# Performance work log

Measured on AMD Instinct MI355X. Metric: run time of the kernel, lower is better.

Reference implementation:

```python
import jax, jax.numpy as jnp
import numpy as np
from jax import lax

K = 3; PAD = 1; STR = 1; DIL = 1; DG = 16; MRM = 10.0


def _conv3(x, w, b):
    y = lax.conv_general_dilated(x, w, (1, 1), ((PAD, PAD), (PAD, PAD)),
                                 dimension_numbers=('NCHW', 'OIHW', 'NCHW'))
    return y + b[None, :, None, None]


def _leaky(x):
    return jnp.where(x >= 0, x, 0.1 * x)


def _bilinear_gather(img, py, px):
    # img: [B, dg, cg, H, W]; py, px: [B, dg, KK, H, W] sampling coords
    B, dg, cg, H, W = img.shape
    KK = py.shape[2]
    y0f = jnp.floor(py); x0f = jnp.floor(px)
    wy = py - y0f; wx = px - x0f          # bilinear fractions (grad flows via py/px)
    y0 = y0f.astype(jnp.int32); x0 = x0f.astype(jnp.int32)
    y1 = y0 + 1; x1 = x0 + 1
    imgf = img.reshape(B * dg, cg, H * W)

    def gather(yi, xi):
        valid = ((yi >= 0) & (yi < H) & (xi >= 0) & (xi < W)).astype(img.dtype)
        idx = jnp.clip(yi, 0, H - 1) * W + jnp.clip(xi, 0, W - 1)
        idxf = idx.reshape(B * dg, KK * H * W)
        v = jax.vmap(lambda im, ix: im[:, ix])(imgf, idxf)  # [B*dg, cg, KK*H*W]
        v = v.reshape(B, dg, cg, KK, H, W)
        return v * valid[:, :, None]  # zero padding outside image

    w00 = ((1 - wy) * (1 - wx))[:, :, None]
    w01 = ((1 - wy) * wx)[:, :, None]
    w10 = (wy * (1 - wx))[:, :, None]
    w11 = (wy * wx)[:, :, None]
    return (gather(y0, x0) * w00 + gather(y0, x1) * w01 +
            gather(y1, x0) * w10 + gather(y1, x1) * w11)


def reference(x, extra_feat, flow, w1, b1, w2, b2, w3, b3, weight):
    B, C, H, W = x.shape
    KK = K * K
    cg = C // DG
    P = DG * KK
    # offset/mask generating convnet
    h = _leaky(_conv3(extra_feat, w1, b1))
    h = _leaky(_conv3(h, w2, b2))
    o = _conv3(h, w3, b3)                       # [B, 3*P, H, W]
    o1, o2, m = jnp.split(o, 3, axis=1)
    off = MRM * jnp.tanh(jnp.concatenate([o1, o2], axis=1))  # [B, 2P, H, W]
    flow_yx = flow[:, ::-1]                      # flip(1): (x,y)->(y,x)
    off = off + jnp.tile(flow_yx, (1, P, 1, 1))
    off = off.reshape(B, DG, KK, 2, H, W)        # pair p=(g,k): channel 2p=y, 2p+1=x
    off_y = off[:, :, :, 0]
    off_x = off[:, :, :, 1]
    mask = jax.nn.sigmoid(m).reshape(B, DG, KK, H, W)

    ki = jnp.arange(KK)
    ky = (ki // K).astype(x.dtype) * DIL - PAD   # kernel row offsets
    kx = (ki % K).astype(x.dtype) * DIL - PAD
    base_h = jnp.arange(H, dtype=x.dtype) * STR
    base_w = jnp.arange(W, dtype=x.dtype) * STR
    py = base_h[None, None, None, :, None] + ky[None, None, :, None, None] + off_y
    px = base_w[None, None, None, None, :] + kx[None, None, :, None, None] + off_x

    img = x.reshape(B, DG, cg, H, W)
    val = _bilinear_gather(img, py, px) * mask[:, :, None]  # [B,dg,cg,KK,H,W]
    wk = weight.reshape(weight.shape[0], DG, cg, KK)
    # modulated deformable conv accumulate (bias=None in original forward)
    return jnp.einsum('bgckhw,ogck->bohw', val, wk)


def setup_inputs() -> dict:
    key = jax.random.key(0)
    ks = jax.random.split(key, 10)
    B, C, H, W = 2, 64, 128, 128
    OFFC = 3 * K * K * DG  # 432
    return {
        'x': jax.random.normal(ks[0], (B, C, H, W), jnp.float32),
        'extra_feat': jax.random.normal(ks[1], (B, 2 * C, H, W), jnp.float32),
        'flow': jax.random.normal(ks[2], (B, 2, H, W), jnp.float32),
        'w1': jax.random.normal(ks[3], (C, 2 * C, 3, 3), jnp.float32) * 0.05,
        'b1': jnp.zeros((C,), jnp.float32),
        'w2': jax.random.normal(ks[4], (C, C, 3, 3), jnp.float32) * 0.05,
        'b2': jnp.zeros((C,), jnp.float32),
        'w3': jax.random.normal(ks[5], (OFFC, C, 3, 3), jnp.float32) * 0.01,
        'b3': jnp.zeros((OFFC,), jnp.float32),
        'weight': jax.random.normal(ks[6], (C, C, 3, 3), jnp.float32) * 0.05,
    }
```

## Files before the change

kernel.cpp:

```cpp
#include <hip/hip_runtime.h>
#include <math.h>

constexpr int B_   = 2;
constexpr int C_   = 64;
constexpr int H_   = 128;
constexpr int W_   = 128;
constexpr int HW_  = H_ * W_;
constexpr int DG_  = 16;
constexpr int KK_  = 9;
constexpr int CG_  = 4;
constexpr int OFFC_ = 3 * KK_ * DG_;
constexpr int R_   = C_ * KK_;
constexpr int WP_  = 130;
constexpr int HWP_ = WP_ * WP_;

typedef _Float16 half8 __attribute__((ext_vector_type(8)));
typedef _Float16 half4 __attribute__((ext_vector_type(4)));
typedef float floatx4 __attribute__((ext_vector_type(4)));

__device__ __forceinline__ void gl_lds16(const _Float16* g, _Float16* l)
{
    __builtin_amdgcn_global_load_lds(
        (const __attribute__((address_space(1))) void*)g,
        (__attribute__((address_space(3))) void*)l, 16, 0, 0);
}

__device__ __forceinline__ int afrag_src(int c)
{
    const int cmf = c >> 6, cq = (c >> 4) & 3, cl = c & 15;
    return (cmf * 16 + cl) * 32 + cq * 8;
}

template <int OC, int CIN>
__global__ __launch_bounds__(256) void prep_wA_k(
    const float* __restrict__ w, _Float16* __restrict__ wA)
{
    constexpr int CH = CIN / 32;
    const int j = blockIdx.x * 256 + threadIdx.x;
    if (j >= 9 * CH * OC * 32) return;
    const int slab = j / (OC * 32);
    const int rem  = j - slab * (OC * 32);
    const int oc   = rem >> 5;
    const int jj   = rem & 31;
    const int t    = slab / CH;
    const int h    = slab - t * CH;
    const int ic   = h * 32 + jj;
    wA[j] = (_Float16)w[(size_t)oc * (CIN * 9) + ic * 9 + t];
}

__global__ __launch_bounds__(256) void prep_wkA_k(
    const float* __restrict__ wk, _Float16* __restrict__ wkA)
{
    const int j = blockIdx.x * 256 + threadIdx.x;
    if (j >= 18 * 64 * 32) return;
    const int s   = j >> 11;
    const int rem = j & 2047;
    const int oc  = rem >> 5;
    const int jj  = rem & 31;
    const int k   = s >> 1;
    const int gc  = (s & 1) * 32 + jj;
    wkA[j] = (_Float16)wk[(size_t)oc * R_ + gc * 9 + k];
}

template <int CC>
__global__ __launch_bounds__(256) void nchw2slabpad_f16_k(
    const float* __restrict__ in, _Float16* __restrict__ outh)
{
    const int pix = blockIdx.x * 256 + threadIdx.x;
    const int b   = blockIdx.y;
    const int yp  = pix >> 7;
    const int xp  = pix & (W_ - 1);
    const float* ib = in + (size_t)b * CC * HW_ + pix;
#pragma unroll
    for (int c0 = 0; c0 < CC; c0 += 8) {
        half8 v;
#pragma unroll
        for (int j = 0; j < 8; ++j)
            v[j] = (_Float16)ib[(size_t)(c0 + j) * HW_];
        const int slab = c0 >> 5;
        *(half8*)&outh[((size_t)(slab * B_ + b) * HWP_
                        + (size_t)(yp + 1) * WP_ + (xp + 1)) * 32 + (c0 & 31)] = v;
    }
}

__global__ __launch_bounds__(256) void nchw2gx_f16_k(
    const float* __restrict__ in, _Float16* __restrict__ outh)
{
    const int pix = blockIdx.x * 256 + threadIdx.x;
    const int b   = blockIdx.y;
    const float* ib = in + (size_t)b * C_ * HW_ + pix;
#pragma unroll
    for (int g = 0; g < DG_; ++g) {
        half4 v;
#pragma unroll
        for (int c = 0; c < 4; ++c)
            v[c] = (_Float16)ib[(size_t)(g * 4 + c) * HW_];
        *(half4*)&outh[((size_t)(b * DG_ + g) * HW_ + pix) * 4] = v;
    }
}

__global__ __launch_bounds__(256, 2) void conv1_mfma_k(
    const _Float16* __restrict__ inp, const _Float16* __restrict__ wA,
    const float* __restrict__ bias, _Float16* __restrict__ outp)
{
    __shared__ __align__(16) _Float16 Asm[2 * 4096];

    const int tid  = threadIdx.x;
    const int lane = tid & 63;
    const int wv   = tid >> 6;
    const int l15  = lane & 15;
    const int quad = lane >> 4;

    const int zx   = blockIdx.x;
    const int row  = zx >> 1;
    const int b    = row >> 7;
    const int y    = row & 127;
    const int px0  = (zx & 1) * 64 + wv * 16;

    const int sA = afrag_src(tid);

    floatx4 acc[4];
#pragma unroll
    for (int mf = 0; mf < 4; ++mf)
        acc[mf] = (floatx4){0.f, 0.f, 0.f, 0.f};

    half8 Bf[2][2];

    gl_lds16(wA + 0 * 2048 + sA, Asm + 0 * 2048 + tid * 8);
    gl_lds16(wA + 1 * 2048 + sA, Asm + 1 * 2048 + tid * 8);
#pragma unroll
    for (int j = 0; j < 2; ++j)
        Bf[0][j] = *(const half8*)&inp[
            ((size_t)(j * B_ + b) * HWP_ + (size_t)(y + 0) * WP_
             + (px0 + l15 + 0)) * 32 + quad * 8];
    __syncthreads();

#pragma unroll
    for (int p = 0; p < 18; ++p) {
        const int cur = p & 1, nxt = cur ^ 1;
        if (p < 17) {
            const int ks0 = 2 * p + 2;
            const int t = ks0 >> 2;
            const int h0 = ks0 & 3;
            const int dy = t / 3, dx = t % 3;
#pragma unroll
            for (int j = 0; j < 2; ++j) {
                gl_lds16(wA + (size_t)(ks0 + j) * 2048 + sA,
                         Asm + (nxt * 2 + j) * 2048 + tid * 8);
                Bf[nxt][j] = *(const half8*)&inp[
                    ((size_t)((h0 + j) * B_ + b) * HWP_ + (size_t)(y + dy) * WP_
                     + (px0 + l15 + dx)) * 32 + quad * 8];
            }
        }
#pragma unroll
        for (int j = 0; j < 2; ++j) {
            const _Float16* abase = Asm + (cur * 2 + j) * 2048 + lane * 8;
#pragma unroll
            for (int mf = 0; mf < 4; ++mf) {
                const half8 afr = *(const half8*)&abase[mf * 512];
                acc[mf] = __builtin_amdgcn_mfma_f32_16x16x32_f16(afr, Bf[cur][j], acc[mf], 0, 0, 0);
            }
        }
        __syncthreads();
    }

#pragma unroll
    for (int mf = 0; mf < 4; ++mf) {
        const int oc4 = mf * 16 + quad * 4;
        const float4 b4 = *(const float4*)&bias[oc4];
        half4 v4;
#pragma unroll
        for (int reg = 0; reg < 4; ++reg) {
            float r = acc[mf][reg] + ((const float*)&b4)[reg];
            r = (r >= 0.f) ? r : 0.1f * r;
            v4[reg] = (_Float16)r;
        }
        *(half4*)&outp[((size_t)((oc4 >> 5) * B_ + b) * HWP_
                        + (size_t)(y + 1) * WP_ + (px0 + l15 + 1)) * 32 + (oc4 & 31)] = v4;
    }
}

__global__ __launch_bounds__(256, 2) void conv2_mfma_k(
    const _Float16* __restrict__ inp, const _Float16* __restrict__ wA,
    const float* __restrict__ bias, _Float16* __restrict__ outp)
{
    __shared__ __align__(16) _Float16 Asm[18 * 2048];

    const int tid  = threadIdx.x;
    const int lane = tid & 63;
    const int wv   = tid >> 6;
    const int l15  = lane & 15;
    const int quad = lane >> 4;

    const int zx   = blockIdx.x;
    const int row  = zx >> 1;
    const int b    = row >> 7;
    const int y    = row & 127;
    const int px0  = (zx & 1) * 64 + wv * 16;

    const int sA = afrag_src(tid);

#pragma unroll
    for (int s = 0; s < 18; ++s)
        gl_lds16(wA + (size_t)s * 2048 + sA, Asm + s * 2048 + tid * 8);

    floatx4 acc[4];
#pragma unroll
    for (int mf = 0; mf < 4; ++mf)
        acc[mf] = (floatx4){0.f, 0.f, 0.f, 0.f};

    half8 Bf[2];
    Bf[0] = *(const half8*)&inp[
        ((size_t)(0 * B_ + b) * HWP_ + (size_t)(y + 0) * WP_
         + (px0 + l15 + 0)) * 32 + quad * 8];
    __syncthreads();

#pragma unroll
    for (int ks = 0; ks < 18; ++ks) {
        const int cur = ks & 1, nxt = cur ^ 1;
        if (ks < 17) {
            const int ks1 = ks + 1;
            const int t = ks1 >> 1, h = ks1 & 1;
            const int dy = t / 3, dx = t % 3;
            Bf[nxt] = *(const half8*)&inp[
                ((size_t)(h * B_ + b) * HWP_ + (size_t)(y + dy) * WP_
                 + (px0 + l15 + dx)) * 32 + quad * 8];
        }
        const _Float16* abase = Asm + ks * 2048 + lane * 8;
#pragma unroll
        for (int mf = 0; mf < 4; ++mf) {
            const half8 afr = *(const half8*)&abase[mf * 512];
            acc[mf] = __builtin_amdgcn_mfma_f32_16x16x32_f16(afr, Bf[cur], acc[mf], 0, 0, 0);
        }
    }

#pragma unroll
    for (int mf = 0; mf < 4; ++mf) {
        const int oc4 = mf * 16 + quad * 4;
        const float4 b4 = *(const float4*)&bias[oc4];
        half4 v4;
#pragma unroll
        for (int reg = 0; reg < 4; ++reg) {
            float r = acc[mf][reg] + ((const float*)&b4)[reg];
            r = (r >= 0.f) ? r : 0.1f * r;
            v4[reg] = (_Float16)r;
        }
        *(half4*)&outp[((size_t)((oc4 >> 5) * B_ + b) * HWP_
                        + (size_t)(y + 1) * WP_ + (px0 + l15 + 1)) * 32 + (oc4 & 31)] = v4;
    }
}

__global__ __launch_bounds__(256, 2) void conv3_mfma_k(
    const _Float16* __restrict__ h2p, const _Float16* __restrict__ w3A,
    const float* __restrict__ bias, const float* __restrict__ flow,
    _Float16* __restrict__ omh)
{
    __shared__ __align__(16) _Float16 Smem[144 * 132];
    _Float16* Asm = Smem;
    _Float16* Lds = Smem;

    const int tid  = threadIdx.x;
    const int lane = tid & 63;
    const int wv   = tid >> 6;
    const int l15  = lane & 15;
    const int quad = lane >> 4;

    const int row = blockIdx.x;
    const int b   = row >> 7;
    const int y   = row & 127;
    const int m0  = blockIdx.y * 144;
    const int px0 = wv * 32;

    const int c0 = wv * 64 + lane;
    const int c1 = 256 + c0;
    const int c2 = 512 + lane;
    const int s0 = afrag_src(c0), s1 = afrag_src(c1), s2 = afrag_src(c2);

    floatx4 acc[9][2];
#pragma unroll
    for (int mf = 0; mf < 9; ++mf)
#pragma unroll
        for (int nf = 0; nf < 2; ++nf)
            acc[mf][nf] = (floatx4){0.f, 0.f, 0.f, 0.f};

    half8 Bf[2][2][2];

    {
#pragma unroll
        for (int j = 0; j < 2; ++j) {
            const _Float16* asrc = w3A + ((size_t)j * OFFC_ + m0) * 32;
            _Float16* adst = Asm + j * 4608;
            gl_lds16(asrc + s0, adst + c0 * 8);
            gl_lds16(asrc + s1, adst + c1 * 8);
            if (wv == 0) gl_lds16(asrc + s2, adst + c2 * 8);
#pragma unroll
            for (int nf = 0; nf < 2; ++nf)
                Bf[0][j][nf] = *(const half8*)&h2p[
                    ((size_t)(j * B_ + b) * HWP_ + (size_t)(y + 0) * WP_
                     + (px0 + nf * 16 + l15 + 0)) * 32 + quad * 8];
        }
    }
    __syncthreads();

#pragma unroll
    for (int p = 0; p < 9; ++p) {
        const int cur = p & 1, nxt = cur ^ 1;
        if (p < 8) {
            const int t = p + 1;
            const int dy = t / 3, dx = t % 3;
#pragma unroll
            for (int j = 0; j < 2; ++j) {
                const int ks = 2 * t + j;
                const _Float16* asrc = w3A + ((size_t)ks * OFFC_ + m0) * 32;
                _Float16* adst = Asm + (nxt * 2 + j) * 4608;
                gl_lds16(asrc + s0, adst + c0 * 8);
                gl_lds16(asrc + s1, adst + c1 * 8);
                if (wv == 0) gl_lds16(asrc + s2, adst + c2 * 8);
#pragma unroll
                for (int nf = 0; nf < 2; ++nf)
                    Bf[nxt][j][nf] = *(const half8*)&h2p[
                        ((size_t)(j * B_ + b) * HWP_ + (size_t)(y + dy) * WP_
                         + (px0 + nf * 16 + l15 + dx)) * 32 + quad * 8];
            }
        }
#pragma unroll
        for (int j = 0; j < 2; ++j) {
            const _Float16* abase = Asm + (cur * 2 + j) * 4608 + lane * 8;
#pragma unroll
            for (int mf = 0; mf < 9; ++mf) {
                const half8 afr = *(const half8*)&abase[mf * 512];
                acc[mf][0] = __builtin_amdgcn_mfma_f32_16x16x32_f16(afr, Bf[cur][j][0], acc[mf][0], 0, 0, 0);
                acc[mf][1] = __builtin_amdgcn_mfma_f32_16x16x32_f16(afr, Bf[cur][j][1], acc[mf][1], 0, 0, 0);
            }
        }
        __syncthreads();
    }

    const bool is_off = (blockIdx.y < 2);
    float flY[2], flX[2];
#pragma unroll
    for (int nf = 0; nf < 2; ++nf) {
        const int px = px0 + nf * 16 + l15;
        if (is_off) {
            flY[nf] = flow[(size_t)(b * 2 + 1) * HW_ + y * W_ + px];
            flX[nf] = flow[(size_t)(b * 2 + 0) * HW_ + y * W_ + px];
        }
    }
#pragma unroll
    for (int mf = 0; mf < 9; ++mf) {
        const float4 b4 = *(const float4*)&bias[m0 + mf * 16 + quad * 4];
#pragma unroll
        for (int nf = 0; nf < 2; ++nf) {
            const int px = px0 + nf * 16 + l15;
#pragma unroll
            for (int reg = 0; reg < 4; ++reg) {
                const int ocl = mf * 16 + quad * 4 + reg;
                float val = acc[mf][nf][reg] + ((const float*)&b4)[reg];
                if (is_off) {
                    const int slot = reg & 1;
                    const float fl = slot ? flX[nf] : flY[nf];
                    const float e = __expf(2.f * val);
                    val = 10.f * (1.f - __fdividef(2.f, e + 1.f)) + fl;
                } else {
                    val = __fdividef(1.f, 1.f + __expf(-val));
                }
                Lds[ocl * 132 + px] = (_Float16)val;
            }
        }
    }
    __syncthreads();

#pragma unroll
    for (int it = 0; it < 18; ++it) {
        const int j4 = it * 256 + tid;
        const int r  = j4 >> 5;
        const int c4 = j4 & 31;
        const int oc = m0 + r;
        int g, k, slot;
        if (oc < 2 * DG_ * KK_) {
            g = oc / 18;
            const int rem = oc - g * 18;
            k = rem >> 1;
            slot = rem & 1;
        } else {
            const int c = oc - 2 * DG_ * KK_;
            g = c / 9;
            k = c - g * 9;
            slot = 2;
        }
        const half4 hv = *(const half4*)&Lds[r * 132 + c4 * 4];
        *(half4*)&omh[((size_t)((b * DG_ * KK_ + g * KK_ + k) * 3 + slot)) * HW_
                      + y * W_ + c4 * 4] = hv;
    }
}

__global__ __launch_bounds__(256) void gather_k(
    const _Float16* __restrict__ xg, const _Float16* __restrict__ omh,
    _Float16* __restrict__ valh)
{
    const int tid = threadIdx.x;
    const int pix = blockIdx.x * 256 + tid;
    const int zy  = blockIdx.y;
    const int b   = zy / KK_;
    const int k   = zy - b * KK_;
    const int yp  = pix >> 7;
    const int xp  = pix & (W_ - 1);
    const float fy = (float)(yp + (k / 3) - 1);
    const float fx = (float)(xp + (k % 3) - 1);

    half4 rec[16];
#pragma unroll
    for (int g = 0; g < DG_; ++g) {
        const size_t obase = ((size_t)((b * DG_ + g) * KK_ + k) * 3) * HW_ + pix;
        const float oy = (float)omh[obase];
        const float ox = (float)omh[obase + HW_];
        const float m  = (float)omh[obase + 2 * HW_];

        const float py = fy + oy;
        const float px = fx + ox;
        const float y0f = floorf(py);
        const float x0f = floorf(px);
        const float wy = py - y0f;
        const float wx = px - x0f;
        const int y0 = (int)y0f, x0 = (int)x0f;
        const int y1 = y0 + 1,  x1 = x0 + 1;
        const bool vy0 = ((unsigned)y0 < (unsigned)H_);
        const bool vy1 = ((unsigned)y1 < (unsigned)H_);
        const bool vx0 = ((unsigned)x0 < (unsigned)W_);
        const bool vx1 = ((unsigned)x1 < (unsigned)W_);
        const float w00 = vy0 && vx0 ? (1.f - wy) * (1.f - wx) : 0.f;
        const float w01 = vy0 && vx1 ? (1.f - wy) * wx         : 0.f;
        const float w10 = vy1 && vx0 ? wy * (1.f - wx)         : 0.f;
        const float w11 = vy1 && vx1 ? wy * wx                 : 0.f;
        const int i00 = (vy0 && vx0) ? y0 * W_ + x0 : 0;
        const int i01 = (vy0 && vx1) ? y0 * W_ + x1 : 0;
        const int i10 = (vy1 && vx0) ? y1 * W_ + x0 : 0;
        const int i11 = (vy1 && vx1) ? y1 * W_ + x1 : 0;

        const _Float16* xb = xg + (size_t)(b * DG_ + g) * HW_ * 4;
        const half4 p00 = *(const half4*)&xb[(size_t)i00 * 4];
        const half4 p01 = *(const half4*)&xb[(size_t)i01 * 4];
        const half4 p10 = *(const half4*)&xb[(size_t)i10 * 4];
        const half4 p11 = *(const half4*)&xb[(size_t)i11 * 4];

        half4 v4;
#pragma unroll
        for (int c = 0; c < CG_; ++c) {
            float v = w00 * (float)p00[c] + w01 * (float)p01[c]
                    + w10 * (float)p10[c] + w11 * (float)p11[c];
            v4[c] = (_Float16)(v * m);
        }
        rec[g] = v4;
    }

    _Float16* r0 = &valh[((size_t)((2 * k) * B_ + b) * HW_ + pix) * 32];
    _Float16* r1 = &valh[((size_t)((2 * k + 1) * B_ + b) * HW_ + pix) * 32];
#pragma unroll
    for (int j = 0; j < 4; ++j) {
        half8 w0, w1;
#pragma unroll
        for (int c = 0; c < 4; ++c) {
            w0[c]     = rec[2 * j][c];
            w0[c + 4] = rec[2 * j + 1][c];
            w1[c]     = rec[8 + 2 * j][c];
            w1[c + 4] = rec[9 + 2 * j][c];
        }
        *(half8*)&r0[j * 8] = w0;
        *(half8*)&r1[j * 8] = w1;
    }
}

__global__ __launch_bounds__(256, 2) void einsum_mfma_k(
    const _Float16* __restrict__ valh, const _Float16* __restrict__ wkA,
    float* __restrict__ out)
{
    __shared__ __align__(16) _Float16 Smem[18 * 2048];
    float* Lds = (float*)Smem;

    const int tid  = threadIdx.x;
    const int lane = tid & 63;
    const int wv   = tid >> 6;
    const int l15  = lane & 15;
    const int quad = lane >> 4;

    const int pixg0 = blockIdx.x * 64 + wv * 16;
    const int b     = pixg0 >> 14;
    const int pix0  = pixg0 & (HW_ - 1);

    const int sA = afrag_src(tid);

#pragma unroll
    for (int s = 0; s < 18; ++s)
        gl_lds16(wkA + (size_t)s * 2048 + sA, Smem + s * 2048 + tid * 8);

    floatx4 acc[4];
#pragma unroll
    for (int mf = 0; mf < 4; ++mf)
        acc[mf] = (floatx4){0.f, 0.f, 0.f, 0.f};

    half8 Bf[2];
    Bf[0] = *(const half8*)&valh[((size_t)(0 * B_ + b) * HW_ + pix0 + l15) * 32 + quad * 8];
    __syncthreads();

#pragma unroll
    for (int s = 0; s < 18; ++s) {
        const int cur = s & 1, nxt = cur ^ 1;
        if (s < 17) {
            const int s1 = s + 1;
            Bf[nxt] = *(const half8*)&valh[
                ((size_t)(s1 * B_ + b) * HW_ + pix0 + l15) * 32 + quad * 8];
        }
        const _Float16* abase = Smem + s * 2048 + lane * 8;
#pragma unroll
        for (int mf = 0; mf < 4; ++mf) {
            const half8 afr = *(const half8*)&abase[mf * 512];
            acc[mf] = __builtin_amdgcn_mfma_f32_16x16x32_f16(afr, Bf[cur], acc[mf], 0, 0, 0);
        }
    }
    __syncthreads();

    const int pxl = wv * 16 + l15;
#pragma unroll
    for (int mf = 0; mf < 4; ++mf)
#pragma unroll
        for (int reg = 0; reg < 4; ++reg)
            Lds[(mf * 16 + quad * 4 + reg) * 68 + pxl] = acc[mf][reg];
    __syncthreads();

    const int pixb = blockIdx.x * 64 & (HW_ - 1);
#pragma unroll
    for (int it = 0; it < 4; ++it) {
        const int j4 = it * 256 + tid;
        const int r  = j4 >> 4;
        const int c4 = j4 & 15;
        float4 v;
        v.x = Lds[r * 68 + c4 * 4 + 0];
        v.y = Lds[r * 68 + c4 * 4 + 1];
        v.z = Lds[r * 68 + c4 * 4 + 2];
        v.w = Lds[r * 68 + c4 * 4 + 3];
        *(float4*)&out[((size_t)(b * C_ + r)) * HW_ + pixb + c4 * 4] = v;
    }
}

extern "C" void kernel_launch(void* const* d_in, const int* in_sizes, int n_in,
                              void* d_out, int out_size, void* d_ws, size_t ws_size,
                              hipStream_t stream)
{
    const float* x    = (const float*)d_in[0];
    const float* ef   = (const float*)d_in[1];
    const float* flow = (const float*)d_in[2];
    const float* w1   = (const float*)d_in[3];
    const float* b1   = (const float*)d_in[4];
    const float* w2   = (const float*)d_in[5];
    const float* b2   = (const float*)d_in[6];
    const float* w3   = (const float*)d_in[7];
    const float* b3   = (const float*)d_in[8];
    const float* wk   = (const float*)d_in[9];
    float* out = (float*)d_out;

    _Float16* omh  = (_Float16*)d_ws;
    _Float16* valh = omh + (size_t)B_ * OFFC_ * HW_;
    _Float16* ef_p = valh + (size_t)18 * B_ * HW_ * 32;
    _Float16* xg   = ef_p + (size_t)4 * B_ * HWP_ * 32;
    _Float16* h1p  = xg + (size_t)B_ * HW_ * 64;
    _Float16* h2p  = h1p + (size_t)2 * B_ * HWP_ * 32;
    _Float16* w1A  = h2p + (size_t)2 * B_ * HWP_ * 32;
    _Float16* w2A  = w1A + 64 * 128 * 9;
    _Float16* w3A  = w2A + 64 * 64 * 9;
    _Float16* wkA  = w3A + OFFC_ * 64 * 9;

    hipMemsetAsync(ef_p, 0, (size_t)4 * B_ * HWP_ * 32 * 2, stream);
    hipMemsetAsync(h1p, 0, (size_t)2 * B_ * HWP_ * 32 * 2, stream);
    hipMemsetAsync(h2p, 0, (size_t)2 * B_ * HWP_ * 32 * 2, stream);

    prep_wA_k<64, 128><<<dim3((64 * 128 * 9 + 255) / 256), 256, 0, stream>>>(w1, w1A);
    prep_wA_k<64, 64><<<dim3((64 * 64 * 9 + 255) / 256), 256, 0, stream>>>(w2, w2A);
    prep_wA_k<OFFC_, 64><<<dim3((OFFC_ * 64 * 9 + 255) / 256), 256, 0, stream>>>(w3, w3A);
    prep_wkA_k<<<dim3((18 * 64 * 32 + 255) / 256), 256, 0, stream>>>(wk, wkA);
    nchw2slabpad_f16_k<128><<<dim3(HW_ / 256, B_), 256, 0, stream>>>(ef, ef_p);
    nchw2gx_f16_k<<<dim3(HW_ / 256, B_), 256, 0, stream>>>(x, xg);

    conv1_mfma_k<<<dim3(B_ * H_ * 2), 256, 0, stream>>>(ef_p, w1A, b1, h1p);
    conv2_mfma_k<<<dim3(B_ * H_ * 2), 256, 0, stream>>>(h1p, w2A, b2, h2p);
    conv3_mfma_k<<<dim3(B_ * H_, 3), 256, 0, stream>>>(h2p, w3A, b3, flow, omh);

    gather_k<<<dim3(HW_ / 256, B_ * KK_), 256, 0, stream>>>(xg, omh, valh);
    einsum_mfma_k<<<dim3(B_ * HW_ / 64), 256, 0, stream>>>(valh, wkA, out);
}
```

Baseline: 206.3 us.

## Split conv3 output channels into 48-wide tiles and preload all weights to LDS

```diff
diff --git a/kernel.cpp b/kernel.cpp
--- a/kernel.cpp
+++ b/kernel.cpp
@@ -250,13 +250,12 @@
     }
 }
 
-__global__ __launch_bounds__(256, 2) void conv3_mfma_k(
+__global__ __launch_bounds__(256, 3) void conv3_mfma_k(
     const _Float16* __restrict__ h2p, const _Float16* __restrict__ w3A,
     const float* __restrict__ bias, const float* __restrict__ flow,
     _Float16* __restrict__ omh)
 {
-    __shared__ __align__(16) _Float16 Smem[144 * 132];
-    _Float16* Asm = Smem;
+    __shared__ __align__(16) _Float16 Smem[17 * 1536];
     _Float16* Lds = Smem;
 
     const int tid  = threadIdx.x;
@@ -268,75 +267,71 @@
     const int row = blockIdx.x;
     const int b   = row >> 7;
     const int y   = row & 127;
-    const int m0  = blockIdx.y * 144;
+    const int m0  = blockIdx.y * 48;
     const int px0 = wv * 32;
 
-    const int c0 = wv * 64 + lane;
-    const int c1 = 256 + c0;
-    const int c2 = 512 + lane;
-    const int s0 = afrag_src(c0), s1 = afrag_src(c1), s2 = afrag_src(c2);
-
-    floatx4 acc[9][2];
-#pragma unroll
-    for (int mf = 0; mf < 9; ++mf)
+#pragma unroll
+    for (int r = 0; r < 13; ++r) {
+        const int c = r * 256 + tid;
+        if (c < 17 * 192) {
+            const int ks = c / 192;
+            const int cl = c - ks * 192;
+            const int cmf = cl >> 6, cq = (cl >> 4) & 3, ccl = cl & 15;
+            const _Float16* src = w3A
+                + ((size_t)ks * OFFC_ + m0 + cmf * 16 + ccl) * 32 + cq * 8;
+            gl_lds16(src, Smem + c * 8);
+        }
+    }
+
+    half8 Af17[3];
+#pragma unroll
+    for (int mf = 0; mf < 3; ++mf)
+        Af17[mf] = *(const half8*)&w3A[
+            ((size_t)17 * OFFC_ + m0 + mf * 16 + l15) * 32 + quad * 8];
+
+    floatx4 acc[3][2];
+#pragma unroll
+    for (int mf = 0; mf < 3; ++mf)
 #pragma unroll
         for (int nf = 0; nf < 2; ++nf)
             acc[mf][nf] = (floatx4){0.f, 0.f, 0.f, 0.f};
 
-    half8 Bf[2][2][2];
-
-    {
-#pragma unroll
-        for (int j = 0; j < 2; ++j) {
-            const _Float16* asrc = w3A + ((size_t)j * OFFC_ + m0) * 32;
-            _Float16* adst = Asm + j * 4608;
-            gl_lds16(asrc + s0, adst + c0 * 8);
-            gl_lds16(asrc + s1, adst + c1 * 8);
-            if (wv == 0) gl_lds16(asrc + s2, adst + c2 * 8);
+    half8 Bf[2][2];
+#pragma unroll
+    for (int nf = 0; nf < 2; ++nf)
+        Bf[0][nf] = *(const half8*)&h2p[
+            ((size_t)(0 * B_ + b) * HWP_ + (size_t)(y + 0) * WP_
+             + (px0 + nf * 16 + l15 + 0)) * 32 + quad * 8];
+
+    __syncthreads();
+
+#pragma unroll
+    for (int ks = 0; ks < 18; ++ks) {
+        const int cur = ks & 1, nxt = cur ^ 1;
+        if (ks < 17) {
+            const int ks1 = ks + 1;
+            const int t = ks1 >> 1, h = ks1 & 1;
+            const int dy = t / 3, dx = t % 3;
 #pragma unroll
             for (int nf = 0; nf < 2; ++nf)
-                Bf[0][j][nf] = *(const half8*)&h2p[
-                    ((size_t)(j * B_ + b) * HWP_ + (size_t)(y + 0) * WP_
-                     + (px0 + nf * 16 + l15 + 0)) * 32 + quad * 8];
-        }
-    }
-    __syncthreads();
-
-#pragma unroll
-    for (int p = 0; p < 9; ++p) {
-        const int cur = p & 1, nxt = cur ^ 1;
-        if (p < 8) {
-            const int t = p + 1;
-            const int dy = t / 3, dx = t % 3;
-#pragma unroll
-            for (int j = 0; j < 2; ++j) {
-                const int ks = 2 * t + j;
-                const _Float16* asrc = w3A + ((size_t)ks * OFFC_ + m0) * 32;
-                _Float16* adst = Asm + (nxt * 2 + j) * 4608;
-                gl_lds16(asrc + s0, adst + c0 * 8);
-                gl_lds16(asrc + s1, adst + c1 * 8);
-                if (wv == 0) gl_lds16(asrc + s2, adst + c2 * 8);
-#pragma unroll
-                for (int nf = 0; nf < 2; ++nf)
-                    Bf[nxt][j][nf] = *(const half8*)&h2p[
-                        ((size_t)(j * B_ + b) * HWP_ + (size_t)(y + dy) * WP_
-                         + (px0 + nf * 16 + l15 + dx)) * 32 + quad * 8];
-            }
-        }
-#pragma unroll
-        for (int j = 0; j < 2; ++j) {
-            const _Float16* abase = Asm + (cur * 2 + j) * 4608 + lane * 8;
-#pragma unroll
-            for (int mf = 0; mf < 9; ++mf) {
-                const half8 afr = *(const half8*)&abase[mf * 512];
-                acc[mf][0] = __builtin_amdgcn_mfma_f32_16x16x32_f16(afr, Bf[cur][j][0], acc[mf][0], 0, 0, 0);
-                acc[mf][1] = __builtin_amdgcn_mfma_f32_16x16x32_f16(afr, Bf[cur][j][1], acc[mf][1], 0, 0, 0);
-            }
-        }
-        __syncthreads();
-    }
-
-    const bool is_off = (blockIdx.y < 2);
+                Bf[nxt][nf] = *(const half8*)&h2p[
+                    ((size_t)(h * B_ + b) * HWP_ + (size_t)(y + dy) * WP_
+                     + (px0 + nf * 16 + l15 + dx)) * 32 + quad * 8];
+        }
+#pragma unroll
+        for (int mf = 0; mf < 3; ++mf) {
+            half8 afr;
+            if (ks < 17)
+                afr = *(const half8*)&Smem[ks * 1536 + mf * 512 + lane * 8];
+            else
+                afr = Af17[mf];
+            acc[mf][0] = __builtin_amdgcn_mfma_f32_16x16x32_f16(afr, Bf[cur][0], acc[mf][0], 0, 0, 0);
+            acc[mf][1] = __builtin_amdgcn_mfma_f32_16x16x32_f16(afr, Bf[cur][1], acc[mf][1], 0, 0, 0);
+        }
+    }
+    __syncthreads();
+
+    const bool is_off = (blockIdx.y < 6);
     float flY[2], flX[2];
 #pragma unroll
     for (int nf = 0; nf < 2; ++nf) {
@@ -347,7 +342,7 @@
         }
     }
 #pragma unroll
-    for (int mf = 0; mf < 9; ++mf) {
+    for (int mf = 0; mf < 3; ++mf) {
         const float4 b4 = *(const float4*)&bias[m0 + mf * 16 + quad * 4];
 #pragma unroll
         for (int nf = 0; nf < 2; ++nf) {
@@ -371,7 +366,7 @@
     __syncthreads();
 
 #pragma unroll
-    for (int it = 0; it < 18; ++it) {
+    for (int it = 0; it < 6; ++it) {
         const int j4 = it * 256 + tid;
         const int r  = j4 >> 5;
         const int c4 = j4 & 31;
@@ -582,7 +577,7 @@
 
     conv1_mfma_k<<<dim3(B_ * H_ * 2), 256, 0, stream>>>(ef_p, w1A, b1, h1p);
     conv2_mfma_k<<<dim3(B_ * H_ * 2), 256, 0, stream>>>(h1p, w2A, b2, h2p);
-    conv3_mfma_k<<<dim3(B_ * H_, 3), 256, 0, stream>>>(h2p, w3A, b3, flow, omh);
+    conv3_mfma_k<<<dim3(B_ * H_, 9), 256, 0, stream>>>(h2p, w3A, b3, flow, omh);
 
     gather_k<<<dim3(HW_ / 256, B_ * KK_), 256, 0, stream>>>(xg, omh, valh);
     einsum_mfma_k<<<dim3(B_ * HW_ / 64), 256, 0, stream>>>(valh, wkA, out);
```

New measurement: 208.2 us. About the same (+1.0%).
